# Kernel tuning notes

Measured on AMD Instinct MI355X. Metric: run time of the kernel, lower is better.

The kernel has to match this reference:

```python
import math
import jax, jax.numpy as jnp
import numpy as np

D_EMBD = 1024
N_HEAD = 16
BLOCK = 2048
B, T = 4, 2048


def setup_inputs() -> dict:
    key = jax.random.key(0)
    ks = jax.random.split(key, 5)
    d = D_EMBD
    return {
        "x": jax.random.normal(ks[0], (B, T, d), dtype=jnp.float32),
        "Wq": jax.random.normal(ks[1], (d, d), dtype=jnp.float32),
        "bq": jnp.zeros((d,), dtype=jnp.float32),
        "Wk": jax.random.normal(ks[2], (d, d), dtype=jnp.float32),
        "bk": jnp.zeros((d,), dtype=jnp.float32),
        "Wv": jax.random.normal(ks[3], (d, d), dtype=jnp.float32),
        "bv": jnp.zeros((d,), dtype=jnp.float32),
        "Wp": jax.random.normal(ks[4], (d, d), dtype=jnp.float32),
        "bp": jnp.zeros((d,), dtype=jnp.float32),
    }


def reference(x, Wq, bq, Wk, bk, Wv, bv, Wp, bp):
    Bb, Tt, C = x.shape
    n_head = N_HEAD
    hd = C // n_head  # head dim
    # QKV projections -> [B, H, T, hd]
    def split_heads(y):
        return y.reshape(Bb, Tt, n_head, hd).transpose(0, 2, 1, 3)
    Q = split_heads(x @ Wq + bq)
    K = split_heads(x @ Wk + bk)
    V = split_heads(x @ Wv + bv)
    # scores [B, H, T, T]
    attn = jnp.einsum('bhqd,bhkd->bhqk', Q, K) / math.sqrt(hd)
    # causal mask: -inf strictly above diagonal (matches triu(ones*-inf, 1))
    causal = jnp.tril(jnp.ones((Tt, Tt), dtype=bool))
    attn = jnp.where(causal, attn, -jnp.inf)
    attn = jax.nn.softmax(attn, axis=-1)
    y = jnp.einsum('bhqk,bhkd->bhqd', attn, V)
    y = y.transpose(0, 2, 1, 3).reshape(Bb, Tt, C)
    return y @ Wp + bp
```

## Files before the change

### kernel.cpp

```cpp
#include <hip/hip_runtime.h>
#include <stdint.h>
#include <stddef.h>

#define TT 2048
#define CC 1024
#define BBATCH 4
#define HH 16
#define HD 64
#define MTOT (BBATCH * TT)

typedef __bf16 bf16_t;
typedef __bf16 bf16x4 __attribute__((ext_vector_type(4)));
typedef __bf16 bf16x8 __attribute__((ext_vector_type(8)));
typedef float f32x4 __attribute__((ext_vector_type(4)));

typedef const __attribute__((address_space(1))) uint32_t* as1_u32p;
typedef __attribute__((address_space(3))) uint32_t* as3_u32p;

__device__ __forceinline__ f32x4 mfma16(bf16x8 a, bf16x8 b, f32x4 c) {
  return __builtin_amdgcn_mfma_f32_16x16x32_bf16(a, b, c, 0, 0, 0);
}

__device__ __forceinline__ void gload_lds16(void* lds, const void* g) {
  __builtin_amdgcn_global_load_lds((as1_u32p)g, (as3_u32p)lds, 16, 0, 0);
}

__device__ __forceinline__ bf16x8 rd32(const char* t, int row, int lane) {
  int sl = (lane >> 4) ^ ((row >> 1) & 3);
  return *(const bf16x8*)(t + row * 64 + sl * 16);
}
__device__ __forceinline__ bf16x8 rd64(const char* t, int row, int kk, int lane) {
  int sl = ((lane >> 4) + kk * 4) ^ (row & 7);
  return *(const bf16x8*)(t + row * 128 + sl * 16);
}

__global__ void split_x_kernel(const float* __restrict__ x, bf16_t* __restrict__ xh,
                               bf16_t* __restrict__ xl, int n4) {
  int stride = gridDim.x * blockDim.x;
  for (int i = blockIdx.x * blockDim.x + threadIdx.x; i < n4; i += stride) {
    float4 v = ((const float4*)x)[i];
    float vv[4] = {v.x, v.y, v.z, v.w};
    bf16x4 hv, lv;
#pragma unroll
    for (int j = 0; j < 4; ++j) {
      bf16_t h = (bf16_t)vv[j];
      hv[j] = h;
      lv[j] = (bf16_t)(vv[j] - (float)h);
    }
    *(bf16x4*)(xh + (size_t)i * 4) = hv;
    *(bf16x4*)(xl + (size_t)i * 4) = lv;
  }
}

__global__ void transpose_split_kernel(const float* __restrict__ Wq, const float* __restrict__ Wk,
                                       const float* __restrict__ Wv, const float* __restrict__ Wp,
                                       bf16_t* __restrict__ wqkh, bf16_t* __restrict__ wqkl,
                                       bf16_t* __restrict__ wv_t, bf16_t* __restrict__ wp_t) {
  __shared__ float tile[32][33];
  int mat = blockIdx.z;
  const float* W = (mat == 0) ? Wq : (mat == 1) ? Wk : (mat == 2) ? Wv : Wp;
  int tx = threadIdx.x, ty = threadIdx.y;
  int n0 = blockIdx.x * 32, k0 = blockIdx.y * 32;
#pragma unroll
  for (int j = 0; j < 32; j += 8)
    tile[ty + j][tx] = W[(size_t)(k0 + ty + j) * CC + n0 + tx];
  __syncthreads();
#pragma unroll
  for (int j = 0; j < 32; j += 8) {
    float v = tile[tx][ty + j];
    int n = n0 + ty + j, k = k0 + tx;
    if (mat <= 1) {
      bf16_t h = (bf16_t)v;
      size_t o = (size_t)(mat * CC + n) * CC + k;
      wqkh[o] = h;
      wqkl[o] = (bf16_t)(v - (float)h);
    } else {
      bf16_t* dst = (mat == 2) ? wv_t : wp_t;
      dst[(size_t)n * CC + k] = (bf16_t)v;
    }
  }
}

__global__ __launch_bounds__(512, 2) void gemm_qk_kernel(
    const bf16_t* __restrict__ Ah, const bf16_t* __restrict__ Al,
    const bf16_t* __restrict__ Bh, const bf16_t* __restrict__ Bl,
    const float* __restrict__ bq, const float* __restrict__ bk,
    bf16_t* __restrict__ qh, bf16_t* __restrict__ ql,
    bf16_t* __restrict__ kh, bf16_t* __restrict__ kl) {
  __shared__ __align__(16) char s_ah[2][16384];
  __shared__ __align__(16) char s_al[2][16384];
  __shared__ __align__(16) char s_bh[2][16384];
  __shared__ __align__(16) char s_bl[2][16384];

  const int blk = blockIdx.x;
  const int bn = blk & 7;
  const int bm = blk >> 3;
  const int tid = threadIdx.x, w = tid >> 6, lane = tid & 63;
  const int wr = w >> 2, wc = w & 3;
  const int qi = lane & 15, hi = lane >> 4;

  const int c0 = w * 2, c1 = w * 2 + 1;
  const int srow0 = c0 * 16 + (lane >> 2);
  const int srow1 = c1 * 16 + (lane >> 2);
  const int ssl0 = (lane & 3) ^ ((srow0 >> 1) & 3);
  const int ssl1 = (lane & 3) ^ ((srow1 >> 1) & 3);
  const size_t a_off0 = (size_t)(bm * 256 + srow0) * CC + ssl0 * 8;
  const size_t a_off1 = (size_t)(bm * 256 + srow1) * CC + ssl1 * 8;
  const size_t b_off0 = (size_t)(bn * 256 + srow0) * CC + ssl0 * 8;
  const size_t b_off1 = (size_t)(bn * 256 + srow1) * CC + ssl1 * 8;

  f32x4 acc[8][4] = {};

#define STAGE_QK(buf, k0)                                        \
  do {                                                           \
    gload_lds16(s_ah[buf] + c0 * 1024, Ah + a_off0 + (k0));      \
    gload_lds16(s_ah[buf] + c1 * 1024, Ah + a_off1 + (k0));      \
    gload_lds16(s_al[buf] + c0 * 1024, Al + a_off0 + (k0));      \
    gload_lds16(s_al[buf] + c1 * 1024, Al + a_off1 + (k0));      \
    gload_lds16(s_bh[buf] + c0 * 1024, Bh + b_off0 + (k0));      \
    gload_lds16(s_bh[buf] + c1 * 1024, Bh + b_off1 + (k0));      \
    gload_lds16(s_bl[buf] + c0 * 1024, Bl + b_off0 + (k0));      \
    gload_lds16(s_bl[buf] + c1 * 1024, Bl + b_off1 + (k0));      \
  } while (0)

  STAGE_QK(0, 0);
  int cur = 0;
  for (int ks = 0; ks < 32; ++ks) {
    if (ks < 31) {
      STAGE_QK(cur ^ 1, (ks + 1) * 32);
      asm volatile("s_waitcnt vmcnt(8)" ::: "memory");
    } else {
      asm volatile("s_waitcnt vmcnt(0)" ::: "memory");
    }
    __builtin_amdgcn_s_barrier();

    bf16x8 bfh[4], bfl[4];
#pragma unroll
    for (int ni = 0; ni < 4; ++ni) {
      int br = wc * 64 + ni * 16 + qi;
      bfh[ni] = rd32(s_bh[cur], br, lane);
      bfl[ni] = rd32(s_bl[cur], br, lane);
    }
    __builtin_amdgcn_s_setprio(1);
#pragma unroll
    for (int mi = 0; mi < 8; ++mi) {
      int ar = wr * 128 + mi * 16 + qi;
      bf16x8 ahf = rd32(s_ah[cur], ar, lane);
      bf16x8 alf = rd32(s_al[cur], ar, lane);
#pragma unroll
      for (int ni = 0; ni < 4; ++ni) {
        acc[mi][ni] = mfma16(ahf, bfh[ni], acc[mi][ni]);
        acc[mi][ni] = mfma16(ahf, bfl[ni], acc[mi][ni]);
        acc[mi][ni] = mfma16(alf, bfh[ni], acc[mi][ni]);
      }
    }
    __builtin_amdgcn_s_setprio(0);
    asm volatile("s_waitcnt lgkmcnt(0)" ::: "memory");
    __builtin_amdgcn_s_barrier();
    cur ^= 1;
  }
#undef STAGE_QK

  const int which = bn >> 2;
  const float* bias = which ? bk : bq;
  bf16_t* oh = which ? kh : qh;
  bf16_t* ol = which ? kl : ql;
#pragma unroll
  for (int mi = 0; mi < 8; ++mi) {
#pragma unroll
    for (int ni = 0; ni < 4; ++ni) {
      const int col = bn * 256 + wc * 64 + ni * 16 + qi;
      const int c1i = col & 1023;
      const int h = c1i >> 6, d = c1i & 63;
#pragma unroll
      for (int r = 0; r < 4; ++r) {
        const int row = bm * 256 + wr * 128 + mi * 16 + hi * 4 + r;
        const int b = row >> 11, t = row & 2047;
        float v = acc[mi][ni][r] + bias[c1i];
        if (!which) v *= 0.125f;
        const size_t off = ((size_t)(b * HH + h) * TT + t) * HD + d;
        bf16_t hv = (bf16_t)v;
        oh[off] = hv;
        ol[off] = (bf16_t)(v - (float)hv);
      }
    }
  }
}

template <int MODE>
__global__ __launch_bounds__(256) void gemm_kernel(
    const bf16_t* __restrict__ Ah,
    const bf16_t* __restrict__ Bh,
    const float* __restrict__ bias0,
    void* __restrict__ out0) {
  __shared__ __align__(16) char smem[2 * 8192];
  char* sAh = smem;
  char* sBh = smem + 8192;

  const int bn = blockIdx.x, bm = blockIdx.y;
  const int tid = threadIdx.x, w = tid >> 6, lane = tid & 63;
  const int wr = w >> 1, wc = w & 1;

  f32x4 acc[4][4] = {};

  for (int ks = 0; ks < 32; ++ks) {
    const int k0 = ks * 32;
    __syncthreads();
#pragma unroll
    for (int it = 0; it < 2; ++it) {
      int c = it * 4 + w;
      int row = c * 16 + (lane >> 2);
      int sl = (lane & 3) ^ ((row >> 1) & 3);
      size_t aoff = (size_t)(bm * 128 + row) * CC + k0 + sl * 8;
      size_t boff = (size_t)(bn * 128 + row) * CC + k0 + sl * 8;
      gload_lds16(sAh + c * 1024, Ah + aoff);
      gload_lds16(sBh + c * 1024, Bh + boff);
    }
    __syncthreads();

    bf16x8 afh[4], bfh[4];
#pragma unroll
    for (int i = 0; i < 4; ++i) {
      int ar = wr * 64 + i * 16 + (lane & 15);
      int br = wc * 64 + i * 16 + (lane & 15);
      afh[i] = rd32(sAh, ar, lane);
      bfh[i] = rd32(sBh, br, lane);
    }
#pragma unroll
    for (int mi = 0; mi < 4; ++mi) {
#pragma unroll
      for (int ni = 0; ni < 4; ++ni) {
        acc[mi][ni] = mfma16(afh[mi], bfh[ni], acc[mi][ni]);
      }
    }
  }

#pragma unroll
  for (int mi = 0; mi < 4; ++mi) {
#pragma unroll
    for (int ni = 0; ni < 4; ++ni) {
      const int col = bn * 128 + wc * 64 + ni * 16 + (lane & 15);
#pragma unroll
      for (int r = 0; r < 4; ++r) {
        const int row = bm * 128 + wr * 64 + mi * 16 + (lane >> 4) * 4 + r;
        float v = acc[mi][ni][r];
        if (MODE == 1) {
          const int h = col >> 6, d = col & 63;
          const int b = row >> 11, t = row & 2047;
          float vv = v + bias0[col];
          ((bf16_t*)out0)[((size_t)(b * HH + h) * HD + d) * TT + t] = (bf16_t)vv;
        } else {
          ((float*)out0)[(size_t)row * CC + col] = v + bias0[col];
        }
      }
    }
  }
}

__global__ __launch_bounds__(512, 4) void attn_kernel(
    const bf16_t* __restrict__ qh, const bf16_t* __restrict__ ql,
    const bf16_t* __restrict__ kh, const bf16_t* __restrict__ kl,
    const bf16_t* __restrict__ vt, bf16_t* __restrict__ y) {
  __shared__ __align__(16) char s_kh[2][8192];
  __shared__ __align__(16) char s_kl[2][8192];
  __shared__ __align__(16) char s_vt[2][8192];
  __shared__ __align__(16) char s_p[8][2048];

  const int blk = blockIdx.x;
  const int bh = (blk & 7) * 8 + ((blk >> 3) & 7);
  const int p = blk >> 6;
  const int b = bh >> 4, h = bh & 15;
  const int tid = threadIdx.x, w = tid >> 6, lane = tid & 63;
  const int hi = lane >> 4, qi = lane & 15;

  const int st_row = w * 8 + (lane >> 3);
  const int st_sl = (lane & 7) ^ (st_row & 7);
  const size_t st_koff0 = ((size_t)bh * TT + st_row) * HD + st_sl * 8;
  const size_t st_voff0 = ((size_t)bh * HD + st_row) * TT + st_sl * 8;

#pragma unroll
  for (int half = 0; half < 2; ++half) {
    const int qb = half ? (15 - p) : p;
    const int ktmax = 2 * qb + 1;
    const int qrow0 = qb * 128 + w * 16;
    const int qv = qrow0 + qi;

    bf16x8 qhf[2], qlf[2];
#pragma unroll
    for (int kk = 0; kk < 2; ++kk) {
      size_t off = ((size_t)bh * TT + qrow0 + qi) * HD + kk * 32 + hi * 8;
      qhf[kk] = *(const bf16x8*)(qh + off);
      qlf[kk] = *(const bf16x8*)(ql + off);
    }

    f32x4 o[4] = {};
    float m = -1e30f, l = 0.f;

    gload_lds16(s_kh[0] + w * 1024, kh + st_koff0);
    gload_lds16(s_kl[0] + w * 1024, kl + st_koff0);
    gload_lds16(s_vt[0] + w * 1024, vt + st_voff0);

    int cur = 0;
    for (int kt = 0; kt <= ktmax; ++kt) {
      if (kt < ktmax) {
        const size_t koff = st_koff0 + (size_t)(kt + 1) * 64 * HD;
        const size_t voff = st_voff0 + (size_t)(kt + 1) * 64;
        gload_lds16(s_kh[cur ^ 1] + w * 1024, kh + koff);
        gload_lds16(s_kl[cur ^ 1] + w * 1024, kl + koff);
        gload_lds16(s_vt[cur ^ 1] + w * 1024, vt + voff);
        asm volatile("s_waitcnt vmcnt(3)" ::: "memory");
      } else {
        asm volatile("s_waitcnt vmcnt(0)" ::: "memory");
      }
      __builtin_amdgcn_s_barrier();

      const char* ckh = s_kh[cur];
      const char* ckl = s_kl[cur];
      const char* cvt = s_vt[cur];
      const bool active = (qrow0 + 15 >= kt * 64);
      if (active) {
        f32x4 st[4];
#pragma unroll
        for (int cf = 0; cf < 4; ++cf) {
          f32x4 s = {};
#pragma unroll
          for (int kk = 0; kk < 2; ++kk) {
            bf16x8 kfh = rd64(ckh, cf * 16 + qi, kk, lane);
            bf16x8 kfl = rd64(ckl, cf * 16 + qi, kk, lane);
            s = mfma16(kfh, qhf[kk], s);
            s = mfma16(kfl, qhf[kk], s);
            s = mfma16(kfh, qlf[kk], s);
          }
          st[cf] = s;
        }

        if (kt * 64 + 63 > qrow0) {
#pragma unroll
          for (int cf = 0; cf < 4; ++cf)
#pragma unroll
            for (int r = 0; r < 4; ++r)
              if (kt * 64 + cf * 16 + hi * 4 + r > qv) st[cf][r] = -1e30f;
        }

        float tmax = st[0][0];
#pragma unroll
        for (int cf = 0; cf < 4; ++cf)
#pragma unroll
          for (int r = 0; r < 4; ++r) tmax = fmaxf(tmax, st[cf][r]);
        tmax = fmaxf(tmax, __shfl_xor(tmax, 16));
        tmax = fmaxf(tmax, __shfl_xor(tmax, 32));
        const float mnew = fmaxf(m, tmax);
        const float sc = __expf(m - mnew);
        float ps = 0.f;
#pragma unroll
        for (int cf = 0; cf < 4; ++cf) {
          bf16x4 pp;
#pragma unroll
          for (int r = 0; r < 4; ++r) {
            float pv = __expf(st[cf][r] - mnew);
            ps += pv;
            pp[r] = (bf16_t)pv;
          }
          int slot = ((cf << 1) + (hi >> 1)) ^ (qi & 7);
          *(bf16x4*)(&s_p[w][0] + qi * 128 + slot * 16 + (hi & 1) * 8) = pp;
        }
        ps += __shfl_xor(ps, 16);
        ps += __shfl_xor(ps, 32);
        l = l * sc + ps;
        m = mnew;
#pragma unroll
        for (int cd = 0; cd < 4; ++cd) {
#pragma unroll
          for (int r = 0; r < 4; ++r) o[cd][r] *= sc;
        }

#pragma unroll
        for (int kk = 0; kk < 2; ++kk) {
          bf16x8 pf = rd64(&s_p[w][0], qi, kk, lane);
#pragma unroll
          for (int cd = 0; cd < 4; ++cd) {
            bf16x8 vf = rd64(cvt, cd * 16 + qi, kk, lane);
            o[cd] = mfma16(vf, pf, o[cd]);
          }
        }
      }

      asm volatile("s_waitcnt lgkmcnt(0)" ::: "memory");
      __builtin_amdgcn_s_barrier();
      cur ^= 1;
    }

    const float inv = 1.f / l;
    const int t = qrow0 + qi;
#pragma unroll
    for (int cd = 0; cd < 4; ++cd) {
      bf16x4 ov;
#pragma unroll
      for (int r = 0; r < 4; ++r) ov[r] = (bf16_t)(o[cd][r] * inv);
      *(bf16x4*)(y + (size_t)(b * TT + t) * CC + h * HD + cd * 16 + hi * 4) = ov;
    }
  }
}

extern "C" void kernel_launch(void* const* d_in, const int* in_sizes, int n_in,
                              void* d_out, int out_size, void* d_ws, size_t ws_size,
                              hipStream_t stream) {
  (void)in_sizes; (void)n_in; (void)out_size; (void)ws_size;
  const float* x  = (const float*)d_in[0];
  const float* Wq = (const float*)d_in[1];
  const float* bq = (const float*)d_in[2];
  const float* Wk = (const float*)d_in[3];
  const float* bk = (const float*)d_in[4];
  const float* Wv = (const float*)d_in[5];
  const float* bv = (const float*)d_in[6];
  const float* Wp = (const float*)d_in[7];
  const float* bp = (const float*)d_in[8];

  char* ws = (char*)d_ws;
  const size_t MB = 1024 * 1024;
  bf16_t* xh   = (bf16_t*)(ws + 0 * MB);
  bf16_t* xl   = (bf16_t*)(ws + 16 * MB);
  bf16_t* wqkh = (bf16_t*)(ws + 32 * MB);
  bf16_t* wqkl = (bf16_t*)(ws + 36 * MB);
  bf16_t* wv_t = (bf16_t*)(ws + 40 * MB);
  bf16_t* wp_t = (bf16_t*)(ws + 42 * MB);
  bf16_t* qhw  = (bf16_t*)(ws + 44 * MB);
  bf16_t* qlw  = (bf16_t*)(ws + 60 * MB);
  bf16_t* khw  = (bf16_t*)(ws + 76 * MB);
  bf16_t* klw  = (bf16_t*)(ws + 92 * MB);
  bf16_t* vtw  = (bf16_t*)(ws + 108 * MB);
  bf16_t* yw   = (bf16_t*)(ws + 124 * MB);

  split_x_kernel<<<2048, 256, 0, stream>>>(x, xh, xl, MTOT * CC / 4);
  transpose_split_kernel<<<dim3(32, 32, 4), dim3(32, 8), 0, stream>>>(
      Wq, Wk, Wv, Wp, wqkh, wqkl, wv_t, wp_t);
  gemm_qk_kernel<<<256, 512, 0, stream>>>(
      xh, xl, wqkh, wqkl, bq, bk, qhw, qlw, khw, klw);
  gemm_kernel<1><<<dim3(8, 64), 256, 0, stream>>>(
      xh, wv_t, bv, vtw);
  attn_kernel<<<512, 512, 0, stream>>>(qhw, qlw, khw, klw, vtw, yw);
  gemm_kernel<2><<<dim3(8, 64), 256, 0, stream>>>(
      yw, wp_t, bp, d_out);
}
```

Measured before the change: 250.4 us.

## Interleave QK projection global-to-LDS prefetch with MFMA phases in four sub-stages

Restructures the QK projection GEMM main loop so the next tile's global-to-LDS loads are split into four pairs and issued between four MFMA phases, instead of all at the top of the iteration. A-fragment LDS reads are also software-pipelined two rows at a time. The goal is to spread memory traffic across the compute and overlap it with MFMA work. The cost is many more barriers per k-step, which adds synchronisation overhead. The vmcnt wait now only waits for the earlier loads, which depends on the loads completing in issue order.

```diff
diff --git a/kernel.cpp b/kernel.cpp
--- a/kernel.cpp
+++ b/kernel.cpp
@@ -111,55 +111,108 @@
 
   f32x4 acc[8][4] = {};
 
-#define STAGE_QK(buf, k0)                                        \
-  do {                                                           \
-    gload_lds16(s_ah[buf] + c0 * 1024, Ah + a_off0 + (k0));      \
-    gload_lds16(s_ah[buf] + c1 * 1024, Ah + a_off1 + (k0));      \
-    gload_lds16(s_al[buf] + c0 * 1024, Al + a_off0 + (k0));      \
-    gload_lds16(s_al[buf] + c1 * 1024, Al + a_off1 + (k0));      \
-    gload_lds16(s_bh[buf] + c0 * 1024, Bh + b_off0 + (k0));      \
-    gload_lds16(s_bh[buf] + c1 * 1024, Bh + b_off1 + (k0));      \
-    gload_lds16(s_bl[buf] + c0 * 1024, Bl + b_off0 + (k0));      \
-    gload_lds16(s_bl[buf] + c1 * 1024, Bl + b_off1 + (k0));      \
-  } while (0)
-
-  STAGE_QK(0, 0);
+#define DO_MI(mi, ahf, alf)                                  \
+  {                                                          \
+    _Pragma("unroll") for (int ni = 0; ni < 4; ++ni) {       \
+      acc[mi][ni] = mfma16(ahf, bfh[ni], acc[mi][ni]);       \
+      acc[mi][ni] = mfma16(ahf, bfl[ni], acc[mi][ni]);       \
+      acc[mi][ni] = mfma16(alf, bfh[ni], acc[mi][ni]);       \
+    }                                                        \
+  }
+
+  gload_lds16(s_ah[0] + c0 * 1024, Ah + a_off0);
+  gload_lds16(s_ah[0] + c1 * 1024, Ah + a_off1);
+  gload_lds16(s_al[0] + c0 * 1024, Al + a_off0);
+  gload_lds16(s_al[0] + c1 * 1024, Al + a_off1);
+  gload_lds16(s_bh[0] + c0 * 1024, Bh + b_off0);
+  gload_lds16(s_bh[0] + c1 * 1024, Bh + b_off1);
+  gload_lds16(s_bl[0] + c0 * 1024, Bl + b_off0);
+  gload_lds16(s_bl[0] + c1 * 1024, Bl + b_off1);
+
   int cur = 0;
   for (int ks = 0; ks < 32; ++ks) {
-    if (ks < 31) {
-      STAGE_QK(cur ^ 1, (ks + 1) * 32);
-      asm volatile("s_waitcnt vmcnt(8)" ::: "memory");
+    const int nb = cur ^ 1;
+    const size_t kn = (size_t)(ks + 1) * 32;
+    const bool pre = (ks < 31);
+    const int ar0 = wr * 128 + qi;
+
+    if (pre) {
+      gload_lds16(s_ah[nb] + c0 * 1024, Ah + a_off0 + kn);
+      gload_lds16(s_ah[nb] + c1 * 1024, Ah + a_off1 + kn);
+      asm volatile("s_waitcnt vmcnt(2)" ::: "memory");
     } else {
       asm volatile("s_waitcnt vmcnt(0)" ::: "memory");
     }
     __builtin_amdgcn_s_barrier();
-
     bf16x8 bfh[4], bfl[4];
 #pragma unroll
     for (int ni = 0; ni < 4; ++ni) {
-      int br = wc * 64 + ni * 16 + qi;
+      const int br = wc * 64 + ni * 16 + qi;
       bfh[ni] = rd32(s_bh[cur], br, lane);
       bfl[ni] = rd32(s_bl[cur], br, lane);
     }
+    bf16x8 p0h = rd32(s_ah[cur], ar0 + 0, lane);
+    bf16x8 p0l = rd32(s_al[cur], ar0 + 0, lane);
+    bf16x8 p1h = rd32(s_ah[cur], ar0 + 16, lane);
+    bf16x8 p1l = rd32(s_al[cur], ar0 + 16, lane);
+    asm volatile("s_waitcnt lgkmcnt(0)" ::: "memory");
     __builtin_amdgcn_s_setprio(1);
-#pragma unroll
-    for (int mi = 0; mi < 8; ++mi) {
-      int ar = wr * 128 + mi * 16 + qi;
-      bf16x8 ahf = rd32(s_ah[cur], ar, lane);
-      bf16x8 alf = rd32(s_al[cur], ar, lane);
-#pragma unroll
-      for (int ni = 0; ni < 4; ++ni) {
-        acc[mi][ni] = mfma16(ahf, bfh[ni], acc[mi][ni]);
-        acc[mi][ni] = mfma16(ahf, bfl[ni], acc[mi][ni]);
-        acc[mi][ni] = mfma16(alf, bfh[ni], acc[mi][ni]);
-      }
-    }
+    DO_MI(0, p0h, p0l);
+    DO_MI(1, p1h, p1l);
     __builtin_amdgcn_s_setprio(0);
+    __builtin_amdgcn_s_barrier();
+
+    p0h = rd32(s_ah[cur], ar0 + 32, lane);
+    p0l = rd32(s_al[cur], ar0 + 32, lane);
+    p1h = rd32(s_ah[cur], ar0 + 48, lane);
+    p1l = rd32(s_al[cur], ar0 + 48, lane);
+    if (pre) {
+      gload_lds16(s_al[nb] + c0 * 1024, Al + a_off0 + kn);
+      gload_lds16(s_al[nb] + c1 * 1024, Al + a_off1 + kn);
+    }
+    __builtin_amdgcn_s_barrier();
     asm volatile("s_waitcnt lgkmcnt(0)" ::: "memory");
-    __builtin_amdgcn_s_barrier();
-    cur ^= 1;
-  }
-#undef STAGE_QK
+    __builtin_amdgcn_s_setprio(1);
+    DO_MI(2, p0h, p0l);
+    DO_MI(3, p1h, p1l);
+    __builtin_amdgcn_s_setprio(0);
+    __builtin_amdgcn_s_barrier();
+
+    p0h = rd32(s_ah[cur], ar0 + 64, lane);
+    p0l = rd32(s_al[cur], ar0 + 64, lane);
+    p1h = rd32(s_ah[cur], ar0 + 80, lane);
+    p1l = rd32(s_al[cur], ar0 + 80, lane);
+    if (pre) {
+      gload_lds16(s_bh[nb] + c0 * 1024, Bh + b_off0 + kn);
+      gload_lds16(s_bh[nb] + c1 * 1024, Bh + b_off1 + kn);
+    }
+    __builtin_amdgcn_s_barrier();
+    asm volatile("s_waitcnt lgkmcnt(0)" ::: "memory");
+    __builtin_amdgcn_s_setprio(1);
+    DO_MI(4, p0h, p0l);
+    DO_MI(5, p1h, p1l);
+    __builtin_amdgcn_s_setprio(0);
+    __builtin_amdgcn_s_barrier();
+
+    p0h = rd32(s_ah[cur], ar0 + 96, lane);
+    p0l = rd32(s_al[cur], ar0 + 96, lane);
+    p1h = rd32(s_ah[cur], ar0 + 112, lane);
+    p1l = rd32(s_al[cur], ar0 + 112, lane);
+    if (pre) {
+      gload_lds16(s_bl[nb] + c0 * 1024, Bl + b_off0 + kn);
+      gload_lds16(s_bl[nb] + c1 * 1024, Bl + b_off1 + kn);
+    }
+    __builtin_amdgcn_s_barrier();
+    asm volatile("s_waitcnt lgkmcnt(0)" ::: "memory");
+    __builtin_amdgcn_s_setprio(1);
+    DO_MI(6, p0h, p0l);
+    DO_MI(7, p1h, p1l);
+    __builtin_amdgcn_s_setprio(0);
+    __builtin_amdgcn_s_barrier();
+
+    cur = nb;
+  }
+#undef DO_MI
 
   const int which = bn >> 2;
   const float* bias = which ? bk : bq;
```

Measured after the change: 255.7 us. +2.1%, slower.

## Switch attention to 32x32x16 MFMA with register-resident P and 4-wave blocks

Applied to the files above, without the earlier changes.

Rewrites the attention inner loop to use 32x32x16 bf16 MFMA tiles, with each wave owning 32 query rows instead of 16 and the block shrunk from 8 to 4 waves. The softmax probabilities are now packed straight from the score accumulators into the PV operand registers, which removes the per-wave shared-memory P buffer and its round trip. The K rows are loaded in a permuted order so the accumulator layout matches the B-operand layout. This is meant to cut LDS traffic and instruction count, at the cost of more registers per thread and fewer waves per block.

```diff
diff --git a/kernel.cpp b/kernel.cpp
--- a/kernel.cpp
+++ b/kernel.cpp
@@ -13,12 +13,16 @@
 typedef __bf16 bf16x4 __attribute__((ext_vector_type(4)));
 typedef __bf16 bf16x8 __attribute__((ext_vector_type(8)));
 typedef float f32x4 __attribute__((ext_vector_type(4)));
+typedef float f32x16 __attribute__((ext_vector_type(16)));
 
 typedef const __attribute__((address_space(1))) uint32_t* as1_u32p;
 typedef __attribute__((address_space(3))) uint32_t* as3_u32p;
 
 __device__ __forceinline__ f32x4 mfma16(bf16x8 a, bf16x8 b, f32x4 c) {
   return __builtin_amdgcn_mfma_f32_16x16x32_bf16(a, b, c, 0, 0, 0);
+}
+__device__ __forceinline__ f32x16 mfma32(bf16x8 a, bf16x8 b, f32x16 c) {
+  return __builtin_amdgcn_mfma_f32_32x32x16_bf16(a, b, c, 0, 0, 0);
 }
 
 __device__ __forceinline__ void gload_lds16(void* lds, const void* g) {
@@ -29,9 +33,8 @@
   int sl = (lane >> 4) ^ ((row >> 1) & 3);
   return *(const bf16x8*)(t + row * 64 + sl * 16);
 }
-__device__ __forceinline__ bf16x8 rd64(const char* t, int row, int kk, int lane) {
-  int sl = ((lane >> 4) + kk * 4) ^ (row & 7);
-  return *(const bf16x8*)(t + row * 128 + sl * 16);
+__device__ __forceinline__ bf16x8 rd32r(const char* t, int row, int slot) {
+  return *(const bf16x8*)(t + row * 128 + ((slot ^ (row & 7)) * 16));
 }
 
 __global__ void split_x_kernel(const float* __restrict__ x, bf16_t* __restrict__ xh,
@@ -257,58 +260,67 @@
   }
 }
 
-__global__ __launch_bounds__(512, 4) void attn_kernel(
+__global__ __launch_bounds__(256, 2) void attn_kernel(
     const bf16_t* __restrict__ qh, const bf16_t* __restrict__ ql,
     const bf16_t* __restrict__ kh, const bf16_t* __restrict__ kl,
     const bf16_t* __restrict__ vt, bf16_t* __restrict__ y) {
   __shared__ __align__(16) char s_kh[2][8192];
   __shared__ __align__(16) char s_kl[2][8192];
   __shared__ __align__(16) char s_vt[2][8192];
-  __shared__ __align__(16) char s_p[8][2048];
 
   const int blk = blockIdx.x;
   const int bh = (blk & 7) * 8 + ((blk >> 3) & 7);
   const int p = blk >> 6;
   const int b = bh >> 4, h = bh & 15;
   const int tid = threadIdx.x, w = tid >> 6, lane = tid & 63;
-  const int hi = lane >> 4, qi = lane & 15;
-
-  const int st_row = w * 8 + (lane >> 3);
-  const int st_sl = (lane & 7) ^ (st_row & 7);
-  const size_t st_koff0 = ((size_t)bh * TT + st_row) * HD + st_sl * 8;
-  const size_t st_voff0 = ((size_t)bh * HD + st_row) * TT + st_sl * 8;
+  const int l31 = lane & 31, hi = lane >> 5;
+
+  const int strow0 = w * 16 + (lane >> 3);
+  const int strow1 = strow0 + 8;
+  const int sl0 = (lane & 7) ^ (strow0 & 7);
+  const int sl1 = (lane & 7) ^ (strow1 & 7);
+  const int ksrow0 = (strow0 & ~12) | ((strow0 & 4) << 1) | ((strow0 & 8) >> 1);
+  const int ksrow1 = (strow1 & ~12) | ((strow1 & 4) << 1) | ((strow1 & 8) >> 1);
+  const size_t koff0 = ((size_t)bh * TT + ksrow0) * HD + sl0 * 8;
+  const size_t koff1 = ((size_t)bh * TT + ksrow1) * HD + sl1 * 8;
+  const size_t voff0 = ((size_t)bh * HD + strow0) * TT + sl0 * 8;
+  const size_t voff1 = ((size_t)bh * HD + strow1) * TT + sl1 * 8;
+  const int ch0 = (w * 2) * 1024, ch1 = (w * 2 + 1) * 1024;
+
+#define STAGE_ATTN(buf, kt)                                                  \
+  do {                                                                       \
+    gload_lds16(s_kh[buf] + ch0, kh + koff0 + (size_t)(kt) * 64 * HD);       \
+    gload_lds16(s_kh[buf] + ch1, kh + koff1 + (size_t)(kt) * 64 * HD);       \
+    gload_lds16(s_kl[buf] + ch0, kl + koff0 + (size_t)(kt) * 64 * HD);       \
+    gload_lds16(s_kl[buf] + ch1, kl + koff1 + (size_t)(kt) * 64 * HD);       \
+    gload_lds16(s_vt[buf] + ch0, vt + voff0 + (size_t)(kt) * 64);            \
+    gload_lds16(s_vt[buf] + ch1, vt + voff1 + (size_t)(kt) * 64);            \
+  } while (0)
 
 #pragma unroll
   for (int half = 0; half < 2; ++half) {
     const int qb = half ? (15 - p) : p;
     const int ktmax = 2 * qb + 1;
-    const int qrow0 = qb * 128 + w * 16;
-    const int qv = qrow0 + qi;
-
-    bf16x8 qhf[2], qlf[2];
-#pragma unroll
-    for (int kk = 0; kk < 2; ++kk) {
-      size_t off = ((size_t)bh * TT + qrow0 + qi) * HD + kk * 32 + hi * 8;
-      qhf[kk] = *(const bf16x8*)(qh + off);
-      qlf[kk] = *(const bf16x8*)(ql + off);
-    }
-
-    f32x4 o[4] = {};
+    const int qrow0 = qb * 128 + w * 32;
+    const int qv = qrow0 + l31;
+
+    bf16x8 qhf[4], qlf[4];
+#pragma unroll
+    for (int kc = 0; kc < 4; ++kc) {
+      size_t off = ((size_t)bh * TT + qv) * HD + kc * 16 + hi * 8;
+      qhf[kc] = *(const bf16x8*)(qh + off);
+      qlf[kc] = *(const bf16x8*)(ql + off);
+    }
+
+    f32x16 o0 = {}, o1 = {};
     float m = -1e30f, l = 0.f;
 
-    gload_lds16(s_kh[0] + w * 1024, kh + st_koff0);
-    gload_lds16(s_kl[0] + w * 1024, kl + st_koff0);
-    gload_lds16(s_vt[0] + w * 1024, vt + st_voff0);
-
+    STAGE_ATTN(0, 0);
     int cur = 0;
     for (int kt = 0; kt <= ktmax; ++kt) {
       if (kt < ktmax) {
-        const size_t koff = st_koff0 + (size_t)(kt + 1) * 64 * HD;
-        const size_t voff = st_voff0 + (size_t)(kt + 1) * 64;
-        gload_lds16(s_kh[cur ^ 1] + w * 1024, kh + koff);
-        gload_lds16(s_kl[cur ^ 1] + w * 1024, kl + koff);
-        gload_lds16(s_vt[cur ^ 1] + w * 1024, vt + voff);
-        asm volatile("s_waitcnt vmcnt(3)" ::: "memory");
+        STAGE_ATTN(cur ^ 1, kt + 1);
+        asm volatile("s_waitcnt vmcnt(6)" ::: "memory");
       } else {
         asm volatile("s_waitcnt vmcnt(0)" ::: "memory");
       }
@@ -317,71 +329,72 @@
       const char* ckh = s_kh[cur];
       const char* ckl = s_kl[cur];
       const char* cvt = s_vt[cur];
-      const bool active = (qrow0 + 15 >= kt * 64);
+      const bool active = (qrow0 + 31 >= kt * 64);
       if (active) {
-        f32x4 st[4];
-#pragma unroll
-        for (int cf = 0; cf < 4; ++cf) {
-          f32x4 s = {};
-#pragma unroll
-          for (int kk = 0; kk < 2; ++kk) {
-            bf16x8 kfh = rd64(ckh, cf * 16 + qi, kk, lane);
-            bf16x8 kfl = rd64(ckl, cf * 16 + qi, kk, lane);
-            s = mfma16(kfh, qhf[kk], s);
-            s = mfma16(kfl, qhf[kk], s);
-            s = mfma16(kfh, qlf[kk], s);
+        f32x16 s0 = {}, s1 = {};
+#pragma unroll
+        for (int kc = 0; kc < 4; ++kc) {
+          bf16x8 kfh = rd32r(ckh, l31, kc * 2 + hi);
+          bf16x8 kfl = rd32r(ckl, l31, kc * 2 + hi);
+          s0 = mfma32(kfh, qhf[kc], s0);
+          s0 = mfma32(kfl, qhf[kc], s0);
+          s0 = mfma32(kfh, qlf[kc], s0);
+        }
+#pragma unroll
+        for (int kc = 0; kc < 4; ++kc) {
+          bf16x8 kfh = rd32r(ckh, 32 + l31, kc * 2 + hi);
+          bf16x8 kfl = rd32r(ckl, 32 + l31, kc * 2 + hi);
+          s1 = mfma32(kfh, qhf[kc], s1);
+          s1 = mfma32(kfl, qhf[kc], s1);
+          s1 = mfma32(kfh, qlf[kc], s1);
+        }
+
+        if (kt * 64 + 63 > qrow0) {
+#pragma unroll
+          for (int r = 0; r < 16; ++r) {
+            const int kvb = kt * 64 + (r & 7) + 8 * hi + 16 * (r >> 3);
+            if (kvb > qv) s0[r] = -1e30f;
+            if (kvb + 32 > qv) s1[r] = -1e30f;
           }
-          st[cf] = s;
-        }
-
-        if (kt * 64 + 63 > qrow0) {
-#pragma unroll
-          for (int cf = 0; cf < 4; ++cf)
-#pragma unroll
-            for (int r = 0; r < 4; ++r)
-              if (kt * 64 + cf * 16 + hi * 4 + r > qv) st[cf][r] = -1e30f;
-        }
-
-        float tmax = st[0][0];
-#pragma unroll
-        for (int cf = 0; cf < 4; ++cf)
-#pragma unroll
-          for (int r = 0; r < 4; ++r) tmax = fmaxf(tmax, st[cf][r]);
-        tmax = fmaxf(tmax, __shfl_xor(tmax, 16));
+        }
+
+        float tmax = s0[0];
+#pragma unroll
+        for (int r = 0; r < 16; ++r) {
+          tmax = fmaxf(tmax, s0[r]);
+          tmax = fmaxf(tmax, s1[r]);
+        }
         tmax = fmaxf(tmax, __shfl_xor(tmax, 32));
         const float mnew = fmaxf(m, tmax);
         const float sc = __expf(m - mnew);
         float ps = 0.f;
 #pragma unroll
-        for (int cf = 0; cf < 4; ++cf) {
-          bf16x4 pp;
-#pragma unroll
-          for (int r = 0; r < 4; ++r) {
-            float pv = __expf(st[cf][r] - mnew);
-            ps += pv;
-            pp[r] = (bf16_t)pv;
-          }
-          int slot = ((cf << 1) + (hi >> 1)) ^ (qi & 7);
-          *(bf16x4*)(&s_p[w][0] + qi * 128 + slot * 16 + (hi & 1) * 8) = pp;
-        }
-        ps += __shfl_xor(ps, 16);
+        for (int r = 0; r < 16; ++r) {
+          s0[r] = __expf(s0[r] - mnew);
+          ps += s0[r];
+          s1[r] = __expf(s1[r] - mnew);
+          ps += s1[r];
+        }
         ps += __shfl_xor(ps, 32);
         l = l * sc + ps;
         m = mnew;
 #pragma unroll
-        for (int cd = 0; cd < 4; ++cd) {
-#pragma unroll
-          for (int r = 0; r < 4; ++r) o[cd][r] *= sc;
-        }
-
-#pragma unroll
-        for (int kk = 0; kk < 2; ++kk) {
-          bf16x8 pf = rd64(&s_p[w][0], qi, kk, lane);
-#pragma unroll
-          for (int cd = 0; cd < 4; ++cd) {
-            bf16x8 vf = rd64(cvt, cd * 16 + qi, kk, lane);
-            o[cd] = mfma16(vf, pf, o[cd]);
-          }
+        for (int r = 0; r < 16; ++r) { o0[r] *= sc; o1[r] *= sc; }
+
+        bf16x8 pa[4];
+#pragma unroll
+        for (int cc = 0; cc < 4; ++cc) {
+#pragma unroll
+          for (int j = 0; j < 8; ++j)
+            pa[cc][j] = (bf16_t)((cc >> 1) ? s1[8 * (cc & 1) + j] : s0[8 * (cc & 1) + j]);
+        }
+
+#pragma unroll
+        for (int cc = 0; cc < 4; ++cc) {
+          bf16x8 vf0 = rd32r(cvt, l31, cc * 2 + hi);
+          bf16x8 vf1 = rd32r(cvt, 32 + l31, cc * 2 + hi);
+          o0 = mfma32(vf0, pa[cc], o0);
+          o1 = mfma32(vf1, pa[cc], o1);
         }
       }
 
@@ -391,15 +404,20 @@
     }
 
     const float inv = 1.f / l;
-    const int t = qrow0 + qi;
-#pragma unroll
-    for (int cd = 0; cd < 4; ++cd) {
-      bf16x4 ov;
-#pragma unroll
-      for (int r = 0; r < 4; ++r) ov[r] = (bf16_t)(o[cd][r] * inv);
-      *(bf16x4*)(y + (size_t)(b * TT + t) * CC + h * HD + cd * 16 + hi * 4) = ov;
-    }
-  }
+    bf16_t* yb = y + (size_t)(b * TT + qv) * CC + h * HD;
+#pragma unroll
+    for (int g = 0; g < 4; ++g) {
+      bf16x4 ov0, ov1;
+#pragma unroll
+      for (int r = 0; r < 4; ++r) {
+        ov0[r] = (bf16_t)(o0[g * 4 + r] * inv);
+        ov1[r] = (bf16_t)(o1[g * 4 + r] * inv);
+      }
+      *(bf16x4*)(yb + g * 8 + hi * 4) = ov0;
+      *(bf16x4*)(yb + 32 + g * 8 + hi * 4) = ov1;
+    }
+  }
+#undef STAGE_ATTN
 }
 
 extern "C" void kernel_launch(void* const* d_in, const int* in_sizes, int n_in,
@@ -438,7 +456,7 @@
       xh, xl, wqkh, wqkl, bq, bk, qhw, qlw, khw, klw);
   gemm_kernel<1><<<dim3(8, 64), 256, 0, stream>>>(
       xh, wv_t, bv, vtw);
-  attn_kernel<<<512, 512, 0, stream>>>(qhw, qlw, khw, klw, vtw, yw);
+  attn_kernel<<<512, 256, 0, stream>>>(qhw, qlw, khw, klw, vtw, yw);
   gemm_kernel<2><<<dim3(8, 64), 256, 0, stream>>>(
       yw, wp_t, bp, d_out);
 }
```

New measurement: 248.5 us. About the same (-0.8%).
